# Performance work log

Measured on AMD Instinct MI355X. Metric: run time of the kernel, lower is better.

The kernel has to match this reference:

```python
import jax, jax.numpy as jnp
import numpy as np

N_NODES = 50000
N_EDGES = 800000
IN_DIM = 128
HID_DIM = 64
N_HEADS = 4
OUT_DIM = 128
NEG_SLOPE = 0.2  # DGL GATConv default


def gat_conv(x, src, dst, W, attn_l, attn_r, bias, n_nodes):
    """DGL GATConv forward. x:[N,Fin], W:[Fin,H*D], attn_*:[H,D], bias:[H,D]. Returns [N,H,D]."""
    H, D = attn_l.shape
    h = (x @ W).reshape(n_nodes, H, D)              # [N,H,D]
    el = jnp.sum(h * attn_l[None], axis=-1)          # [N,H]
    er = jnp.sum(h * attn_r[None], axis=-1)          # [N,H]
    e = jax.nn.leaky_relu(el[src] + er[dst], NEG_SLOPE)  # [E,H]
    # edge softmax over incoming edges of each dst node (stable)
    m = jax.ops.segment_max(e, dst, num_segments=n_nodes)   # [N,H], -inf for empty
    ex = jnp.exp(e - m[dst])                                 # [E,H]
    denom = jax.ops.segment_sum(ex, dst, num_segments=n_nodes)  # [N,H]
    alpha = ex / denom[dst]                                  # [E,H]
    out = jax.ops.segment_sum(alpha[:, :, None] * h[src], dst, num_segments=n_nodes)
    return out + bias[None]                                  # [N,H,D]


def setup_inputs() -> dict:
    key = jax.random.key(0)
    ks = jax.random.split(key, 12)
    x = jax.random.normal(ks[0], (N_NODES, IN_DIM), dtype=jnp.float32)
    src = jax.random.randint(ks[1], (N_EDGES,), 0, N_NODES, dtype=jnp.int32)
    dst = jax.random.randint(ks[2], (N_EDGES,), 0, N_NODES, dtype=jnp.int32)
    s1 = 1.0 / np.sqrt(IN_DIM)
    s2 = 1.0 / np.sqrt(HID_DIM * N_HEADS)
    W1 = jax.random.normal(ks[3], (IN_DIM, N_HEADS * HID_DIM), dtype=jnp.float32) * s1
    al1 = jax.random.normal(ks[4], (N_HEADS, HID_DIM), dtype=jnp.float32) * 0.1
    ar1 = jax.random.normal(ks[5], (N_HEADS, HID_DIM), dtype=jnp.float32) * 0.1
    b1 = jnp.zeros((N_HEADS, HID_DIM), dtype=jnp.float32)
    W2 = jax.random.normal(ks[6], (N_HEADS * HID_DIM, OUT_DIM), dtype=jnp.float32) * s2
    al2 = jax.random.normal(ks[7], (1, OUT_DIM), dtype=jnp.float32) * 0.1
    ar2 = jax.random.normal(ks[8], (1, OUT_DIM), dtype=jnp.float32) * 0.1
    b2 = jnp.zeros((1, OUT_DIM), dtype=jnp.float32)
    return {"x": x, "src": src, "dst": dst, "W1": W1, "al1": al1, "ar1": ar1,
            "b1": b1, "W2": W2, "al2": al2, "ar2": ar2, "b2": b2}


def reference(x, src, dst, W1, al1, ar1, b1, W2, al2, ar2, b2):
    n = x.shape[0]
    h1 = gat_conv(x, src, dst, W1, al1, ar1, b1, n)          # [N,H,D]
    h1 = jax.nn.relu(h1).reshape(n, -1)                       # [N,H*D]
    h2 = gat_conv(h1, src, dst, W2, al2, ar2, b2, n)          # [N,1,OUT]
    return h2.reshape(n, -1)                                   # [N,OUT]
```

## Files before the change

### kernel.cpp

```cpp
#include <hip/hip_runtime.h>
#include <hip/hip_bf16.h>
#include <math.h>


#define NEG_SLOPE 0.2f
#define NB 256
#define CH 8192

typedef short short8 __attribute__((ext_vector_type(8)));
typedef float float4v __attribute__((ext_vector_type(4)));
typedef float float2v __attribute__((ext_vector_type(2)));

static __device__ __forceinline__ float lrelu(float v) {
    return v > 0.f ? v : NEG_SLOPE * v;
}

static __device__ __forceinline__ unsigned short f2bf(float f) {
    unsigned int u = __float_as_uint(f);
    u = (u + 0x7fffu + ((u >> 16) & 1u)) >> 16;
    return (unsigned short)u;
}
static __device__ __forceinline__ float bf2f(unsigned int lo16) {
    return __uint_as_float(lo16 << 16);
}

static __device__ __forceinline__ int bucket_of(int d, unsigned int M) {
    return (int)(((unsigned long long)(unsigned int)d * M) >> 32);
}

static __device__ __forceinline__ void pk_step(float2v& a00, float2v& a01,
                                               float2v& a10, float2v& a11,
                                               float2v& d0, float2v& d1,
                                               float4 w, unsigned int v) {
    float2v w01; w01[0] = w.x; w01[1] = w.y;
    float2v w23; w23[0] = w.z; w23[1] = w.w;
    float x0 = __uint_as_float(v << 16);
    float x1 = __uint_as_float(v & 0xffff0000u);
    float2v xx0 = {x0, x0};
    float2v xx1 = {x1, x1};
    asm("v_pk_fma_f32 %0, %1, %2, %0" : "+v"(a00) : "v"(w01), "v"(xx0));
    asm("v_pk_fma_f32 %0, %1, %2, %0" : "+v"(a01) : "v"(w23), "v"(xx0));
    asm("v_pk_fma_f32 %0, %1, %2, %0" : "+v"(a10) : "v"(w01), "v"(xx1));
    asm("v_pk_fma_f32 %0, %1, %2, %0" : "+v"(a11) : "v"(w23), "v"(xx1));
    asm("v_pk_add_f32 %0, %1, %0" : "+v"(d0) : "v"(w01));
    asm("v_pk_add_f32 %0, %1, %0" : "+v"(d1) : "v"(w23));
}


__global__ __launch_bounds__(256) void histbin_kernel(
        const int* __restrict__ dst, int* __restrict__ bcnt,
        int E, unsigned int M, int nblk,
        const float* __restrict__ W1, const float* __restrict__ al1,
        const float* __restrict__ ar1, const float* __restrict__ W2,
        const float* __restrict__ al2, const float* __restrict__ ar2,
        unsigned short* __restrict__ W1th, unsigned short* __restrict__ Qt1,
        unsigned short* __restrict__ Qt2, unsigned short* __restrict__ W2t) {
    int b = blockIdx.x;
    int tid = threadIdx.x;
    if (b < nblk) {
        __shared__ int lcnt[NB];
        lcnt[tid] = 0;
        __syncthreads();
        int e0 = b * CH;
        for (int i = tid; i < CH; i += 256) {
            int e = e0 + i;
            if (e < E) atomicAdd(&lcnt[bucket_of(dst[e], M)], 1);
        }
        __syncthreads();
        bcnt[b * NB + tid] = lcnt[tid];
        return;
    }
    int idx = (b - nblk) * 256 + tid;
    if (idx < 32768) {
        int h = idx >> 13;
        int r = idx & 8191;
        int d = r >> 7, k = r & 127;
        W1th[idx] = f2bf(W1[k * 256 + h * 64 + d]);
    } else if (idx < 34816) {
        int j = idx - 32768;
        int c = j >> 7, k = j & 127;
        float s = 0.f;
        if (c < 8) {
            int h = c & 3;
            const float* av = ((c < 4) ? al1 : ar1) + h * 64;
            const float* wrow = W1 + k * 256 + h * 64;
            #pragma unroll 8
            for (int d = 0; d < 64; ++d) s += wrow[d] * av[d];
        }
        Qt1[j] = f2bf(s);
    } else if (idx < 36864) {
        int j = idx - 34816;
        int c = j >> 7, k = j & 127;
        float s = (c == 0) ? al2[k] : (c == 1) ? ar2[k] : 0.f;
        Qt2[j] = f2bf(s);
    } else if (idx < 69632) {
        int j = idx - 36864;
        int m = j >> 8, k = j & 255;
        W2t[(size_t)m * 256 + k] = f2bf(W2[(size_t)k * 128 + m]);
    }
}


__global__ __launch_bounds__(256) void binscan_kernel(
        const int* __restrict__ bcnt, int* __restrict__ cur0,
        int* __restrict__ bucketStart, int nblk, int E) {
    __shared__ int s[NB];
    int t = threadIdx.x;
    int tot = 0;
    for (int blk = 0; blk < nblk; ++blk) tot += bcnt[blk * NB + t];
    s[t] = tot;
    __syncthreads();
    for (int off = 1; off < NB; off <<= 1) {
        int add = (t >= off) ? s[t - off] : 0;
        __syncthreads();
        s[t] += add;
        __syncthreads();
    }
    const int bs = s[t] - tot;
    bucketStart[t] = bs;
    if (t == NB - 1) bucketStart[NB] = E;
    int run = bs;
    for (int blk = 0; blk < nblk; ++blk) {
        int c = bcnt[blk * NB + t];
        cur0[blk * NB + t] = run;
        run += c;
    }
}


__global__ __launch_bounds__(256) void scatxdots_kernel(
        const int* __restrict__ src, const int* __restrict__ dst,
        const int* __restrict__ cur0,
        uint2* __restrict__ pairs, int E, unsigned int M, int nblk,
        const float* __restrict__ x, const unsigned short* __restrict__ Qt,
        unsigned short* __restrict__ xb,
        float* __restrict__ el, float* __restrict__ er, int N) {
    constexpr int KP = 136;
    __shared__ alignas(16) unsigned char smem[(64 + 16) * KP * 2];
    const int tid = threadIdx.x;
    if (blockIdx.x < (unsigned)nblk) {
        int* cur = (int*)smem;
        const int b = blockIdx.x;
        cur[tid] = cur0[b * NB + tid];
        __syncthreads();
        int e0 = b * CH;
        for (int i = tid; i < CH; i += 256) {
            int e = e0 + i;
            if (e < E) {
                int d = dst[e];
                int bk = bucket_of(d, M);
                int pos = atomicAdd(&cur[bk], 1);
                pairs[pos] = make_uint2((unsigned int)src[e], (unsigned int)d);
            }
        }
        return;
    }
    unsigned short* As = (unsigned short*)smem;
    unsigned short* Bs = As + 64 * KP;
    const int wid = tid >> 6, lane = tid & 63;
    const int r0 = (blockIdx.x - nblk) * 64;
    for (int ch = tid; ch < 64 * 16; ch += 256) {
        int row = ch >> 4, kc = ch & 15;
        int gr = r0 + row;
        short8 v = {};
        if (gr < N) {
            float4 a = *(const float4*)(x + (size_t)gr * 128 + kc * 8);
            float4 b = *(const float4*)(x + (size_t)gr * 128 + kc * 8 + 4);
            v[0] = (short)f2bf(a.x); v[1] = (short)f2bf(a.y);
            v[2] = (short)f2bf(a.z); v[3] = (short)f2bf(a.w);
            v[4] = (short)f2bf(b.x); v[5] = (short)f2bf(b.y);
            v[6] = (short)f2bf(b.z); v[7] = (short)f2bf(b.w);
            *(short8*)(xb + (size_t)gr * 128 + kc * 8) = v;
        }
        *(short8*)(As + row * KP + kc * 8) = v;
    }
    {
        int row = tid >> 4, kc = tid & 15;
        *(short8*)(Bs + row * KP + kc * 8) = *(const short8*)(Qt + row * 128 + kc * 8);
    }
    __syncthreads();
    float4v acc = (float4v){0.f, 0.f, 0.f, 0.f};
    const int lr = lane & 15, lk = (lane >> 4) * 8;
    #pragma unroll
    for (int ks = 0; ks < 128; ks += 32) {
        short8 af = *(const short8*)(As + (wid * 16 + lr) * KP + ks + lk);
        short8 bf_ = *(const short8*)(Bs + lr * KP + ks + lk);
        acc = __builtin_amdgcn_mfma_f32_16x16x32_bf16(af, bf_, acc, 0, 0, 0);
    }
    const int rbase = r0 + wid * 16 + (lane >> 4) * 4;
    #pragma unroll
    for (int j = 0; j < 4; ++j) {
        int row = rbase + j;
        if (row < N) {
            if (lr < 4) el[(size_t)row * 4 + lr] = acc[j];
            else if (lr < 8) er[(size_t)row * 4 + (lr - 4)] = acc[j];
        }
    }
}


__global__ __launch_bounds__(256) void bucketcsr_kernel(
        const uint2* __restrict__ pairs, const int* __restrict__ bucketStart,
        int* __restrict__ row_start, int* __restrict__ srcs,
        int N, int npb, int E) {
    __shared__ int cnt[NB];
    __shared__ int sc[NB];
    int b = blockIdx.x;
    int tid = threadIdx.x;
    int nb0 = b * npb;
    int es = bucketStart[b], ee = bucketStart[b + 1];
    cnt[tid] = 0;
    __syncthreads();
    for (int i = es + tid; i < ee; i += 256) {
        uint2 p = pairs[i];
        atomicAdd(&cnt[(int)p.y - nb0], 1);
    }
    __syncthreads();
    int myc = cnt[tid];
    sc[tid] = myc;
    __syncthreads();
    for (int off = 1; off < NB; off <<= 1) {
        int add = (tid >= off) ? sc[tid - off] : 0;
        __syncthreads();
        sc[tid] += add;
        __syncthreads();
    }
    int excl = sc[tid] - myc;
    int n = nb0 + tid;
    if (n < N && tid < npb) row_start[n] = es + excl;
    if (b == gridDim.x - 1 && tid == 0) row_start[N] = E;
    cnt[tid] = es + excl;
    __syncthreads();
    for (int i = es + tid; i < ee; i += 256) {
        uint2 p = pairs[i];
        int pos = atomicAdd(&cnt[(int)p.y - nb0], 1);
        srcs[pos] = (int)p.x;
    }
}


__global__ __launch_bounds__(256) void agg1x_kernel(const unsigned short* __restrict__ xb,
                            const float* __restrict__ el, const float* __restrict__ er,
                            const int* __restrict__ srcs, const int* __restrict__ row_start,
                            unsigned short* __restrict__ A1, int N) {
    __shared__ int   s_tbl[4][64];
    __shared__ float a_tbl[4][64][4];
    const int wslot = threadIdx.x >> 6;
    const int lane = threadIdx.x & 63;
    const int n = (blockIdx.x * 256 + threadIdx.x) >> 6;
    if (n >= N) return;
    const int rs = row_start[n];
    const int re = row_start[n + 1];

    float2v accP[2][2];
    accP[0][0] = (float2v){0.f, 0.f}; accP[0][1] = (float2v){0.f, 0.f};
    accP[1][0] = (float2v){0.f, 0.f}; accP[1][1] = (float2v){0.f, 0.f};
    float2v dP[2];
    dP[0] = (float2v){0.f, 0.f}; dP[1] = (float2v){0.f, 0.f};

    if (re > rs) {
        const float4 ern = *(const float4*)(er + (size_t)n * 4);
        for (int base = rs; base < re; base += 64) {
            const int cnt = (re - base) < 64 ? (re - base) : 64;
            asm volatile("s_waitcnt lgkmcnt(0)" ::: "memory");
            if (lane < cnt) {
                int sv = srcs[base + lane];
                float4 ev = *(const float4*)(el + (size_t)sv * 4);
                float4 av;
                av.x = __expf(lrelu(ev.x + ern.x));
                av.y = __expf(lrelu(ev.y + ern.y));
                av.z = __expf(lrelu(ev.z + ern.z));
                av.w = __expf(lrelu(ev.w + ern.w));
                s_tbl[wslot][lane] = sv;
                *(float4*)&a_tbl[wslot][lane][0] = av;
            }
            asm volatile("s_waitcnt lgkmcnt(0)" ::: "memory");
            int i = 0;
            for (; i + 4 <= cnt; i += 4) {
                int s0 = s_tbl[wslot][i],     s1 = s_tbl[wslot][i + 1];
                int s2 = s_tbl[wslot][i + 2], s3 = s_tbl[wslot][i + 3];
                float4 w0 = *(const float4*)&a_tbl[wslot][i][0];
                float4 w1 = *(const float4*)&a_tbl[wslot][i + 1][0];
                float4 w2 = *(const float4*)&a_tbl[wslot][i + 2][0];
                float4 w3 = *(const float4*)&a_tbl[wslot][i + 3][0];
                unsigned int v0 = *(const unsigned int*)(xb + (size_t)s0 * 128 + lane * 2);
                unsigned int v1 = *(const unsigned int*)(xb + (size_t)s1 * 128 + lane * 2);
                unsigned int v2 = *(const unsigned int*)(xb + (size_t)s2 * 128 + lane * 2);
                unsigned int v3 = *(const unsigned int*)(xb + (size_t)s3 * 128 + lane * 2);
                pk_step(accP[0][0], accP[0][1], accP[1][0], accP[1][1], dP[0], dP[1], w0, v0);
                pk_step(accP[0][0], accP[0][1], accP[1][0], accP[1][1], dP[0], dP[1], w1, v1);
                pk_step(accP[0][0], accP[0][1], accP[1][0], accP[1][1], dP[0], dP[1], w2, v2);
                pk_step(accP[0][0], accP[0][1], accP[1][0], accP[1][1], dP[0], dP[1], w3, v3);
            }
            for (; i < cnt; ++i) {
                int s0 = s_tbl[wslot][i];
                float4 w = *(const float4*)&a_tbl[wslot][i][0];
                unsigned int v = *(const unsigned int*)(xb + (size_t)s0 * 128 + lane * 2);
                pk_step(accP[0][0], accP[0][1], accP[1][0], accP[1][1], dP[0], dP[1], w, v);
            }
        }
        float i0 = 1.f / dP[0][0], i1 = 1.f / dP[0][1];
        float i2 = 1.f / dP[1][0], i3 = 1.f / dP[1][1];
        accP[0][0][0] *= i0; accP[1][0][0] *= i0;
        accP[0][0][1] *= i1; accP[1][0][1] *= i1;
        accP[0][1][0] *= i2; accP[1][1][0] *= i2;
        accP[0][1][1] *= i3; accP[1][1][1] *= i3;
    }
    unsigned int pk;
    pk = (unsigned int)f2bf(accP[0][0][0]) | ((unsigned int)f2bf(accP[1][0][0]) << 16);
    *(unsigned int*)(A1 + (size_t)n * 512 + 0 * 128 + lane * 2) = pk;
    pk = (unsigned int)f2bf(accP[0][0][1]) | ((unsigned int)f2bf(accP[1][0][1]) << 16);
    *(unsigned int*)(A1 + (size_t)n * 512 + 1 * 128 + lane * 2) = pk;
    pk = (unsigned int)f2bf(accP[0][1][0]) | ((unsigned int)f2bf(accP[1][1][0]) << 16);
    *(unsigned int*)(A1 + (size_t)n * 512 + 2 * 128 + lane * 2) = pk;
    pk = (unsigned int)f2bf(accP[0][1][1]) | ((unsigned int)f2bf(accP[1][1][1]) << 16);
    *(unsigned int*)(A1 + (size_t)n * 512 + 3 * 128 + lane * 2) = pk;
}


__global__ __launch_bounds__(256) void l2fused_kernel(
        const unsigned short* __restrict__ A1,
        const unsigned short* __restrict__ W1th,
        const float* __restrict__ b1,
        const unsigned short* __restrict__ W2t,
        const unsigned short* __restrict__ Qt2,
        unsigned short* __restrict__ h2b,
        float* __restrict__ el2, float* __restrict__ er2,
        int N) {
    constexpr int PP = 72;
    constexpr int KP = 136;
    __shared__ unsigned short Sh[64 * KP];
    const int tid = threadIdx.x;
    const int wid = tid >> 6, lane = tid & 63;
    const int lr = lane & 15, lk = (lane >> 4) * 8;
    const int r0 = blockIdx.x * 64;
    const int arow = r0 + wid * 16 + lr;
    const bool arok = arow < N;
    const int prow = wid * 16 + (lane >> 4) * 4;

    float4v acc2[8];
    #pragma unroll
    for (int cf = 0; cf < 8; ++cf) acc2[cf] = (float4v){0.f, 0.f, 0.f, 0.f};

    for (int h = 0; h < 4; ++h) {
        float4v p[4];
        #pragma unroll
        for (int cf = 0; cf < 4; ++cf) p[cf] = (float4v){0.f, 0.f, 0.f, 0.f};
        const unsigned short* aptr = A1 + (size_t)arow * 512 + h * 128 + lk;
        const unsigned short* w1p  = W1th + h * 8192 + lr * 128 + lk;
        #pragma unroll
        for (int ks = 0; ks < 128; ks += 32) {
            short8 af = {};
            if (arok) af = *(const short8*)(aptr + ks);
            #pragma unroll
            for (int cf = 0; cf < 4; ++cf) {
                short8 bfr = *(const short8*)(w1p + cf * 2048 + ks);
                p[cf] = __builtin_amdgcn_mfma_f32_16x16x32_bf16(af, bfr, p[cf], 0, 0, 0);
            }
        }
        __syncthreads();
        #pragma unroll
        for (int cf = 0; cf < 4; ++cf) {
            float bias = b1[h * 64 + cf * 16 + lr];
            #pragma unroll
            for (int j = 0; j < 4; ++j)
                Sh[(prow + j) * PP + cf * 16 + lr] = f2bf(fmaxf(p[cf][j] + bias, 0.f));
        }
        __syncthreads();
        const unsigned short* w2p = W2t + (size_t)lr * 256 + h * 64 + lk;
        #pragma unroll
        for (int ks2 = 0; ks2 < 64; ks2 += 32) {
            short8 af2 = *(const short8*)(Sh + (wid * 16 + lr) * PP + ks2 + lk);
            #pragma unroll
            for (int cf = 0; cf < 8; ++cf) {
                short8 bf2 = *(const short8*)(w2p + cf * 4096 + ks2);
                acc2[cf] = __builtin_amdgcn_mfma_f32_16x16x32_bf16(af2, bf2, acc2[cf], 0, 0, 0);
            }
        }
    }

    __syncthreads();
    #pragma unroll
    for (int cf = 0; cf < 8; ++cf) {
        int col = cf * 16 + lr;
        #pragma unroll
        for (int j = 0; j < 4; ++j) {
            unsigned short hv = f2bf(acc2[cf][j]);
            int row = prow + j;
            if (r0 + row < N) h2b[(size_t)(r0 + row) * 128 + col] = hv;
            Sh[row * KP + col] = hv;
        }
    }
    __syncthreads();
    float4v dd = (float4v){0.f, 0.f, 0.f, 0.f};
    const unsigned short* qp = Qt2 + lr * 128 + lk;
    #pragma unroll
    for (int ks = 0; ks < 128; ks += 32) {
        short8 af = *(const short8*)(Sh + (wid * 16 + lr) * KP + ks + lk);
        short8 bq = *(const short8*)(qp + ks);
        dd = __builtin_amdgcn_mfma_f32_16x16x32_bf16(af, bq, dd, 0, 0, 0);
    }
    #pragma unroll
    for (int j = 0; j < 4; ++j) {
        int row = r0 + prow + j;
        if (row < N) {
            if (lr == 0) el2[row] = dd[j];
            else if (lr == 1) er2[row] = dd[j];
        }
    }
}


__global__ __launch_bounds__(256) void agg2_kernel(const unsigned short* __restrict__ hb,
                           const float* __restrict__ el, const float* __restrict__ er,
                           const int* __restrict__ srcs, const int* __restrict__ row_start,
                           const float* __restrict__ bias, float* __restrict__ out, int N) {
    __shared__ uint2 t_tbl[4][64];
    const int wslot = threadIdx.x >> 6;
    const int lane = threadIdx.x & 63;
    const int n = (blockIdx.x * 256 + threadIdx.x) >> 6;
    if (n >= N) return;
    const int rs = row_start[n];
    const int re = row_start[n + 1];

    float acc0 = 0.f, acc1 = 0.f, d = 0.f;

    if (re > rs) {
        const float ern = er[n];
        for (int base = rs; base < re; base += 64) {
            const int cnt = (re - base) < 64 ? (re - base) : 64;
            asm volatile("s_waitcnt lgkmcnt(0)" ::: "memory");
            if (lane < cnt) {
                int sv = srcs[base + lane];
                float a = __expf(lrelu(el[sv] + ern));
                t_tbl[wslot][lane] = make_uint2((unsigned int)sv, __float_as_uint(a));
            }
            asm volatile("s_waitcnt lgkmcnt(0)" ::: "memory");
            int i = 0;
            for (; i + 4 <= cnt; i += 4) {
                uint2 t0 = t_tbl[wslot][i],     t1 = t_tbl[wslot][i + 1];
                uint2 t2 = t_tbl[wslot][i + 2], t3 = t_tbl[wslot][i + 3];
                float w0 = __uint_as_float(t0.y), w1 = __uint_as_float(t1.y);
                float w2 = __uint_as_float(t2.y), w3 = __uint_as_float(t3.y);
                unsigned int v0 = *(const unsigned int*)(hb + (size_t)t0.x * 128 + lane * 2);
                unsigned int v1 = *(const unsigned int*)(hb + (size_t)t1.x * 128 + lane * 2);
                unsigned int v2 = *(const unsigned int*)(hb + (size_t)t2.x * 128 + lane * 2);
                unsigned int v3 = *(const unsigned int*)(hb + (size_t)t3.x * 128 + lane * 2);
                d += w0 + w1 + w2 + w3;
                acc0 += w0 * bf2f(v0 & 0xffffu) + w1 * bf2f(v1 & 0xffffu) +
                        w2 * bf2f(v2 & 0xffffu) + w3 * bf2f(v3 & 0xffffu);
                acc1 += w0 * bf2f(v0 >> 16) + w1 * bf2f(v1 >> 16) +
                        w2 * bf2f(v2 >> 16) + w3 * bf2f(v3 >> 16);
            }
            for (; i < cnt; ++i) {
                uint2 t = t_tbl[wslot][i];
                float w = __uint_as_float(t.y);
                unsigned int v = *(const unsigned int*)(hb + (size_t)t.x * 128 + lane * 2);
                d += w;
                acc0 += w * bf2f(v & 0xffffu);
                acc1 += w * bf2f(v >> 16);
            }
        }
        float invd = 1.f / d;
        acc0 *= invd; acc1 *= invd;
    }
    float o0 = acc0 + bias[lane * 2];
    float o1 = acc1 + bias[lane * 2 + 1];
    *(float2*)(out + (size_t)n * 128 + lane * 2) = make_float2(o0, o1);
}


extern "C" void kernel_launch(void* const* d_in, const int* in_sizes, int n_in,
                              void* d_out, int out_size, void* d_ws, size_t ws_size,
                              hipStream_t stream) {
    const float* x   = (const float*)d_in[0];
    const int*   src = (const int*)d_in[1];
    const int*   dst = (const int*)d_in[2];
    const float* W1  = (const float*)d_in[3];
    const float* al1 = (const float*)d_in[4];
    const float* ar1 = (const float*)d_in[5];
    const float* b1  = (const float*)d_in[6];
    const float* W2  = (const float*)d_in[7];
    const float* al2 = (const float*)d_in[8];
    const float* ar2 = (const float*)d_in[9];
    const float* b2  = (const float*)d_in[10];
    float* out = (float*)d_out;

    const int N = in_sizes[0] / 128;
    const int E = in_sizes[1];
    const int npb = (N + NB - 1) / NB;
    const unsigned int M =
        (unsigned int)(((1ULL << 32) + npb - 1) / (unsigned long long)npb);
    const int nblk_e = (E + CH - 1) / CH;

    char* ws = (char*)d_ws;
    size_t oXB   = 0;
    size_t oA1   = oXB + (size_t)N * 128 * 2;
    size_t oH2   = oA1 + (size_t)N * 512 * 2;
    size_t oW1th = oH2 + (size_t)N * 128 * 2;
    size_t oQt1  = oW1th + 32768 * 2;
    size_t oQt2  = oQt1 + 2048 * 2;
    size_t oW2t  = oQt2 + 2048 * 2;
    size_t oEl1  = oW2t + 32768 * 2;
    size_t oEr1  = oEl1 + (size_t)N * 4 * 4;
    size_t oEl2  = oEr1 + (size_t)N * 4 * 4;
    size_t oEr2  = oEl2 + (size_t)N * 4;
    size_t oRow  = oEr2 + (size_t)N * 4;
    size_t oBcnt = oRow + (((size_t)(N + 1) * 4 + 15) & ~(size_t)15);
    size_t oCur0 = oBcnt + (size_t)nblk_e * NB * 4;
    size_t oBkS  = oCur0 + (size_t)nblk_e * NB * 4;
    size_t oPair = (oBkS + (NB + 1) * 4 + 15) & ~(size_t)15;
    size_t oSrcs = oPair + (size_t)E * 8;

    unsigned short* xb   = (unsigned short*)(ws + oXB);
    unsigned short* A1   = (unsigned short*)(ws + oA1);
    unsigned short* h2b  = (unsigned short*)(ws + oH2);
    unsigned short* w1th = (unsigned short*)(ws + oW1th);
    unsigned short* qt1  = (unsigned short*)(ws + oQt1);
    unsigned short* qt2  = (unsigned short*)(ws + oQt2);
    unsigned short* w2t  = (unsigned short*)(ws + oW2t);
    float* el1 = (float*)(ws + oEl1);
    float* er1 = (float*)(ws + oEr1);
    float* el2 = (float*)(ws + oEl2);
    float* er2 = (float*)(ws + oEr2);
    int*   row_start   = (int*)(ws + oRow);
    int*   bcnt        = (int*)(ws + oBcnt);
    int*   cur0        = (int*)(ws + oCur0);
    int*   bucketStart = (int*)(ws + oBkS);
    uint2* pairs       = (uint2*)(ws + oPair);
    int*   srcs        = (int*)(ws + oSrcs);

    const int nrowb = (N + 63) / 64;
    const int nwaveb = (N + 3) / 4;

    histbin_kernel<<<nblk_e + 272, 256, 0, stream>>>(
        dst, bcnt, E, M, nblk_e, W1, al1, ar1, W2, al2, ar2, w1th, qt1, qt2, w2t);

    binscan_kernel<<<1, 256, 0, stream>>>(bcnt, cur0, bucketStart, nblk_e, E);

    scatxdots_kernel<<<nblk_e + nrowb, 256, 0, stream>>>(
        src, dst, cur0, pairs, E, M, nblk_e,
        x, qt1, xb, el1, er1, N);

    bucketcsr_kernel<<<NB, 256, 0, stream>>>(pairs, bucketStart, row_start, srcs, N, npb, E);

    agg1x_kernel<<<nwaveb, 256, 0, stream>>>(xb, el1, er1, srcs, row_start, A1, N);

    l2fused_kernel<<<nrowb, 256, 0, stream>>>(A1, w1th, b1, w2t, qt2, h2b, el2, er2, N);

    agg2_kernel<<<nwaveb, 256, 0, stream>>>(h2b, el2, er2, srcs, row_start, b2, out, N);
}
```

Baseline: 219.4 us.

## Split fused layer-2 projection across waves by head and output columns

```diff
diff --git a/kernel.cpp b/kernel.cpp
--- a/kernel.cpp
+++ b/kernel.cpp
@@ -327,70 +327,94 @@
         unsigned short* __restrict__ h2b,
         float* __restrict__ el2, float* __restrict__ er2,
         int N) {
-    constexpr int PP = 72;
+    constexpr int PW = 264;
     constexpr int KP = 136;
-    __shared__ unsigned short Sh[64 * KP];
+    __shared__ unsigned short Sh[64 * PW];
     const int tid = threadIdx.x;
     const int wid = tid >> 6, lane = tid & 63;
     const int lr = lane & 15, lk = (lane >> 4) * 8;
     const int r0 = blockIdx.x * 64;
-    const int arow = r0 + wid * 16 + lr;
-    const bool arok = arow < N;
-    const int prow = wid * 16 + (lane >> 4) * 4;
-
-    float4v acc2[8];
-    #pragma unroll
-    for (int cf = 0; cf < 8; ++cf) acc2[cf] = (float4v){0.f, 0.f, 0.f, 0.f};
-
-    for (int h = 0; h < 4; ++h) {
-        float4v p[4];
-        #pragma unroll
-        for (int cf = 0; cf < 4; ++cf) p[cf] = (float4v){0.f, 0.f, 0.f, 0.f};
-        const unsigned short* aptr = A1 + (size_t)arow * 512 + h * 128 + lk;
-        const unsigned short* w1p  = W1th + h * 8192 + lr * 128 + lk;
-        #pragma unroll
-        for (int ks = 0; ks < 128; ks += 32) {
-            short8 af = {};
-            if (arok) af = *(const short8*)(aptr + ks);
+    const int prow4 = (lane >> 4) * 4;
+
+    short8 apre[4][4];
+    #pragma unroll
+    for (int rf = 0; rf < 4; ++rf) {
+        int row = r0 + rf * 16 + lr;
+        if (row >= N) row = N - 1;
+        const unsigned short* ap = A1 + (size_t)row * 512 + wid * 128 + lk;
+        #pragma unroll
+        for (int k = 0; k < 4; ++k)
+            apre[rf][k] = *(const short8*)(ap + k * 32);
+    }
+    float bpre[4];
+    #pragma unroll
+    for (int cf = 0; cf < 4; ++cf) bpre[cf] = b1[wid * 64 + cf * 16 + lr];
+
+    float4v p[4][4];
+    #pragma unroll
+    for (int rf = 0; rf < 4; ++rf)
+        #pragma unroll
+        for (int cf = 0; cf < 4; ++cf)
+            p[rf][cf] = (float4v){0.f, 0.f, 0.f, 0.f};
+    const unsigned short* w1p = W1th + wid * 8192 + lr * 128 + lk;
+    #pragma unroll
+    for (int k = 0; k < 4; ++k) {
+        short8 bfr[4];
+        #pragma unroll
+        for (int cf = 0; cf < 4; ++cf)
+            bfr[cf] = *(const short8*)(w1p + cf * 2048 + k * 32);
+        #pragma unroll
+        for (int rf = 0; rf < 4; ++rf)
             #pragma unroll
-            for (int cf = 0; cf < 4; ++cf) {
-                short8 bfr = *(const short8*)(w1p + cf * 2048 + ks);
-                p[cf] = __builtin_amdgcn_mfma_f32_16x16x32_bf16(af, bfr, p[cf], 0, 0, 0);
-            }
-        }
-        __syncthreads();
+            for (int cf = 0; cf < 4; ++cf)
+                p[rf][cf] = __builtin_amdgcn_mfma_f32_16x16x32_bf16(
+                    apre[rf][k], bfr[cf], p[rf][cf], 0, 0, 0);
+    }
+    #pragma unroll
+    for (int rf = 0; rf < 4; ++rf)
         #pragma unroll
         for (int cf = 0; cf < 4; ++cf) {
-            float bias = b1[h * 64 + cf * 16 + lr];
+            float bias = bpre[cf];
             #pragma unroll
             for (int j = 0; j < 4; ++j)
-                Sh[(prow + j) * PP + cf * 16 + lr] = f2bf(fmaxf(p[cf][j] + bias, 0.f));
-        }
-        __syncthreads();
-        const unsigned short* w2p = W2t + (size_t)lr * 256 + h * 64 + lk;
-        #pragma unroll
-        for (int ks2 = 0; ks2 < 64; ks2 += 32) {
-            short8 af2 = *(const short8*)(Sh + (wid * 16 + lr) * PP + ks2 + lk);
+                Sh[(rf * 16 + prow4 + j) * PW + wid * 64 + cf * 16 + lr] =
+                    f2bf(fmaxf(p[rf][cf][j] + bias, 0.f));
+        }
+    __syncthreads();
+
+    float4v acc2[4][2];
+    #pragma unroll
+    for (int rf = 0; rf < 4; ++rf) {
+        acc2[rf][0] = (float4v){0.f, 0.f, 0.f, 0.f};
+        acc2[rf][1] = (float4v){0.f, 0.f, 0.f, 0.f};
+    }
+    const unsigned short* w2p = W2t + (size_t)(wid * 32 + lr) * 256 + lk;
+    #pragma unroll
+    for (int kk = 0; kk < 8; ++kk) {
+        short8 bq0 = *(const short8*)(w2p + kk * 32);
+        short8 bq1 = *(const short8*)(w2p + 16 * 256 + kk * 32);
+        #pragma unroll
+        for (int rf = 0; rf < 4; ++rf) {
+            short8 af = *(const short8*)(Sh + (rf * 16 + lr) * PW + kk * 32 + lk);
+            acc2[rf][0] = __builtin_amdgcn_mfma_f32_16x16x32_bf16(af, bq0, acc2[rf][0], 0, 0, 0);
+            acc2[rf][1] = __builtin_amdgcn_mfma_f32_16x16x32_bf16(af, bq1, acc2[rf][1], 0, 0, 0);
+        }
+    }
+    __syncthreads();
+
+    #pragma unroll
+    for (int rf = 0; rf < 4; ++rf)
+        #pragma unroll
+        for (int cf = 0; cf < 2; ++cf) {
+            int col = wid * 32 + cf * 16 + lr;
             #pragma unroll
-            for (int cf = 0; cf < 8; ++cf) {
-                short8 bf2 = *(const short8*)(w2p + cf * 4096 + ks2);
-                acc2[cf] = __builtin_amdgcn_mfma_f32_16x16x32_bf16(af2, bf2, acc2[cf], 0, 0, 0);
-            }
-        }
-    }
-
-    __syncthreads();
-    #pragma unroll
-    for (int cf = 0; cf < 8; ++cf) {
-        int col = cf * 16 + lr;
-        #pragma unroll
-        for (int j = 0; j < 4; ++j) {
-            unsigned short hv = f2bf(acc2[cf][j]);
-            int row = prow + j;
-            if (r0 + row < N) h2b[(size_t)(r0 + row) * 128 + col] = hv;
-            Sh[row * KP + col] = hv;
-        }
-    }
+            for (int j = 0; j < 4; ++j) {
+                unsigned short hv = f2bf(acc2[rf][cf][j]);
+                int row = rf * 16 + prow4 + j;
+                if (r0 + row < N) h2b[(size_t)(r0 + row) * 128 + col] = hv;
+                Sh[row * KP + col] = hv;
+            }
+        }
     __syncthreads();
     float4v dd = (float4v){0.f, 0.f, 0.f, 0.f};
     const unsigned short* qp = Qt2 + lr * 128 + lk;
@@ -402,7 +426,7 @@
     }
     #pragma unroll
     for (int j = 0; j < 4; ++j) {
-        int row = r0 + prow + j;
+        int row = r0 + wid * 16 + prow4 + j;
         if (row < N) {
             if (lr == 0) el2[row] = dd[j];
             else if (lr == 1) er2[row] = dd[j];
```

Result: faster. 180.0 us (-17.9%).
